# Kernel tuning notes

Measured on AMD Instinct MI355X. Metric: run time of the kernel, lower is better.

Reference implementation:

```python
import jax, jax.numpy as jnp
from jax import lax
import numpy as np

B, T, F = 256, 2048, 12
EV_VOCAB, RS_VOCAB = 32, 8
EED, RED = 6, 3
H, K = 96, 3
D = F + EED + RED  # 21


def setup_inputs() -> dict:
    key = jax.random.key(0)
    ks = jax.random.split(key, 12)
    s = 0.05
    return {
        'seq': jax.random.normal(ks[0], (B, T, F), jnp.float32),
        'ev': jax.random.randint(ks[1], (B, T), 0, EV_VOCAB),
        'rs': jax.random.randint(ks[2], (B, T), 0, RS_VOCAB),
        'lengths': jax.random.randint(ks[3], (B,), 1, T + 1),  # valid lengths in [1, T]
        'event_emb': jax.random.normal(ks[4], (EV_VOCAB, EED), jnp.float32) * s,
        'result_emb': jax.random.normal(ks[5], (RS_VOCAB, RED), jnp.float32) * s,
        'W_ih': jax.random.normal(ks[6], (4 * H, D), jnp.float32) * s,
        'W_hh': jax.random.normal(ks[7], (4 * H, H), jnp.float32) * s,
        'b_ih': jnp.zeros((4 * H,), jnp.float32),
        'b_hh': jnp.zeros((4 * H,), jnp.float32),
        'W_mlp': jax.random.normal(ks[8], (H, H * K), jnp.float32) * s,
        'b_mlp': jnp.zeros((H,), jnp.float32),
        'W_fc': jax.random.normal(ks[9], (2, 2 * H), jnp.float32) * s,
        'b_fc': jnp.zeros((2,), jnp.float32),
    }


def reference(seq, ev, rs, lengths, event_emb, result_emb, W_ih, W_hh, b_ih, b_hh,
              W_mlp, b_mlp, W_fc, b_fc):
    # embed + concat -> [B,T,D]
    x = jnp.concatenate([seq, event_emb[ev], result_emb[rs]], axis=-1)
    xs = jnp.swapaxes(x, 0, 1)  # [T,B,D]
    ts = jnp.arange(T)
    b = b_ih + b_hh

    def step(carry, inp):
        h, c = carry
        x_t, t = inp
        gates = x_t @ W_ih.T + h @ W_hh.T + b  # [B,4H]
        i, f, g, o = jnp.split(gates, 4, axis=-1)  # PyTorch gate order i,f,g,o
        i = jax.nn.sigmoid(i); f = jax.nn.sigmoid(f)
        g = jnp.tanh(g); o = jax.nn.sigmoid(o)
        c_new = f * c + i * g
        h_new = o * jnp.tanh(c_new)
        m = (t < lengths)[:, None]  # packed-seq semantics: freeze state past length
        h = jnp.where(m, h_new, h)
        c = jnp.where(m, c_new, c)
        out = jnp.where(m, h_new, jnp.zeros_like(h_new))  # pad_packed zeros
        return (h, c), out

    h0 = jnp.zeros((B, H), x.dtype)
    (h_fin, _), outs = lax.scan(step, (h0, h0), (xs, ts))
    out_padded = jnp.swapaxes(outs, 0, 1)  # [B,T,H]

    # vectorized last-k gather (replaces torch Python loop)
    idx = lengths[:, None] - K + jnp.arange(K)  # [B,K]
    valid = idx >= 0
    gathered = jnp.take_along_axis(out_padded, jnp.clip(idx, 0)[:, :, None], axis=1)
    gathered = jnp.where(valid[:, :, None], gathered, jnp.zeros_like(gathered))
    lastk = gathered.reshape(B, K * H)

    h_lastk = jax.nn.relu(lastk @ W_mlp.T + b_mlp)
    h = jnp.concatenate([h_fin, h_lastk], axis=1)  # [B,2H]
    return h @ W_fc.T + b_fc  # [B,2]
```

## Files before the change

kernel.cpp:

```cpp
#include <hip/hip_runtime.h>

#define TT 2048
#define FF 12
#define HH 96
#define CH 128
#define NT 768
#define L2E 1.44269504088896340736f

typedef __attribute__((ext_vector_type(2))) float f2;
typedef __attribute__((ext_vector_type(4))) float f4;

__device__ __forceinline__ float fast_exp2(float x){ return __builtin_amdgcn_exp2f(x); }
__device__ __forceinline__ float fast_rcp(float x){ return __builtin_amdgcn_rcpf(x); }

__global__ __launch_bounds__(NT, 3) void lstm_persist(
  const float* __restrict__ seq, const int* __restrict__ ev, const int* __restrict__ rsi,
  const int* __restrict__ len, const float* __restrict__ eemb, const float* __restrict__ remb,
  const float* __restrict__ W_ih, const float* __restrict__ W_hh,
  const float* __restrict__ b_ih, const float* __restrict__ b_hh,
  const float* __restrict__ W_mlp, const float* __restrict__ b_mlp,
  const float* __restrict__ W_fc, const float* __restrict__ b_fc,
  float* __restrict__ out)
{
  const int b   = blockIdx.x;
  const int tid = threadIdx.x;
  const int w   = tid >> 6;
  const int l   = tid & 63;
  const int kh  = l >> 5;
  const int lh  = l & 31;
  const int gt  = lh >> 3;
  const int hq  = lh & 7;
  const int ht  = 8*w + hq;
  const int g   = gt*96 + ht;

  __shared__ __align__(16) float hbuf[2][96];
  __shared__ __align__(16) float xch[CH][32];
  __shared__ __align__(16) float lastk[3*HH];
  __shared__ __align__(16) float tmp[192];
  __shared__ __align__(16) float h2[2*HH];
  __shared__ __align__(16) float et[32*6];
  __shared__ __align__(16) float rt[8*3];
  __shared__ int evb[CH];
  __shared__ int rsb[CH];

  f2 w2[30];
  #pragma unroll
  for (int j = 0; j < 30; ++j) {
    float v0, v1;
    const int c0 = kh*60 + 2*j;
    v0 = (c0 < 96) ? W_hh[g*96 + c0] : ((c0 < 117) ? W_ih[g*21 + (c0-96)] : 0.f);
    const int c1 = c0 + 1;
    v1 = (c1 < 96) ? W_hh[g*96 + c1] : ((c1 < 117) ? W_ih[g*21 + (c1-96)] : 0.f);
    w2[j] = (f2){v0, v1};
  }
  const float bg = b_ih[g] + b_hh[g];

  for (int i = tid; i < 2*HH; i += NT) hbuf[0][i] = 0.f;
  for (int i = tid; i < 3*HH; i += NT) lastk[i] = 0.f;
  for (int i = tid; i < 192;  i += NT) et[i] = eemb[i];
  for (int i = tid; i < 24;   i += NT) rt[i] = remb[i];

  float c_state = 0.f;
  const int L = len[b];

  for (int t0 = 0; t0 < L; t0 += CH) {
    for (int q = tid; q < CH*FF; q += NT) {
      const int r = q / 12;
      const int c = q - r*12;
      xch[r][c] = seq[(size_t)b*(TT*FF) + (size_t)t0*FF + q];
    }
    if (tid < CH) {
      evb[tid] = ev [b*TT + t0 + tid];
      rsb[tid] = rsi[b*TT + t0 + tid];
    }
    __syncthreads();
    for (int q = tid; q < CH*20; q += NT) {
      const int r  = q / 20;
      const int cc = q - r*20 + 12;
      float val;
      if (cc < 18)      val = et[evb[r]*6 + (cc-12)];
      else if (cc < 21) val = rt[rsb[r]*3 + (cc-18)];
      else              val = 0.f;
      xch[r][cc] = val;
    }
    __syncthreads();

    const int nr = min(CH, L - t0);
    for (int r = 0; r < nr; ++r) {
      const int t   = t0 + r;
      const int cur = t & 1;
      const float* hb = &hbuf[cur][0];
      const float* xr = &xch[r][0];
      const f4* A  = (const f4*)(hb + kh*60);
      const f4* Bv = kh ? (const f4*)xr : ((const f4*)hb) + 9;

      f2 acc = (f2){0.f, 0.f};
      #pragma unroll
      for (int j = 0; j < 9; ++j) {
        const f4 q = A[j];
        acc = w2[2*j]   * q.xy + acc;
        acc = w2[2*j+1] * q.zw + acc;
      }
      #pragma unroll
      for (int j = 9; j < 15; ++j) {
        const f4 q = Bv[j-9];
        acc = w2[2*j]   * q.xy + acc;
        acc = w2[2*j+1] * q.zw + acc;
      }
      float p = acc.x + acc.y;
      p += __shfl_xor(p, 32);
      const float s = p + bg;

      const bool is_t = (gt == 2);
      const float arg = is_t ? (-2.f*L2E)*fabsf(s) : (-L2E)*s;
      const float e   = fast_exp2(arg);
      const float r1  = fast_rcp(1.f + e);
      const float a0  = is_t ? copysignf((1.f - e)*r1, s) : r1;

      const float a1 = __shfl_xor(a0, 8);
      const float a2 = __shfl_xor(a0, 16);
      const float a3 = __shfl_xor(a0, 24);
      const float gi = (gt==0) ? a0 : (gt==1) ? a1 : (gt==2) ? a2 : a3;
      const float gf = (gt==1) ? a0 : (gt==0) ? a1 : (gt==3) ? a2 : a3;
      const float gg = (gt==2) ? a0 : (gt==3) ? a1 : (gt==0) ? a2 : a3;
      const float go = (gt==3) ? a0 : (gt==2) ? a1 : (gt==1) ? a2 : a3;

      c_state = fmaf(gf, c_state, gi*gg);
      const float e2 = fast_exp2((-2.f*L2E)*fabsf(c_state));
      const float th = copysignf((1.f - e2)*fast_rcp(1.f + e2), c_state);
      const float hn = go * th;

      if (l < 8) {
        hbuf[cur ^ 1][ht] = hn;
        const int kk = t + 3 - L;
        if (kk >= 0) lastk[kk*96 + ht] = hn;
      }
      __syncthreads();
    }
  }

  const float* hfin = &hbuf[L & 1][0];
  if (tid < 192) {
    const int hh = tid / 96;
    const int m  = tid - hh*96;
    const float* wp = W_mlp + m*288 + hh*144;
    const float* xp = lastk + hh*144;
    float s = 0.f;
    #pragma unroll 8
    for (int i = 0; i < 144; ++i) s = fmaf(wp[i], xp[i], s);
    tmp[tid] = s;
  }
  __syncthreads();
  if (tid < 96) {
    const float hl = tmp[tid] + tmp[96+tid] + b_mlp[tid];
    h2[96 + tid] = fmaxf(hl, 0.f);
    h2[tid] = hfin[tid];
  }
  __syncthreads();
  if (tid < 128) {
    const int o  = tid >> 6;
    const int ll = tid & 63;
    const float* wf = W_fc + o*192 + 3*ll;
    float s = fmaf(wf[0], h2[3*ll+0], fmaf(wf[1], h2[3*ll+1], wf[2]*h2[3*ll+2]));
    #pragma unroll
    for (int off = 32; off > 0; off >>= 1) s += __shfl_down(s, off);
    if (ll == 0) out[b*2 + o] = s + b_fc[o];
  }
}

extern "C" void kernel_launch(void* const* d_in, const int* in_sizes, int n_in,
                              void* d_out, int out_size, void* d_ws, size_t ws_size,
                              hipStream_t stream) {
  const float* seq   = (const float*)d_in[0];
  const int*   ev    = (const int*)  d_in[1];
  const int*   rsi   = (const int*)  d_in[2];
  const int*   len   = (const int*)  d_in[3];
  const float* eemb  = (const float*)d_in[4];
  const float* remb  = (const float*)d_in[5];
  const float* W_ih  = (const float*)d_in[6];
  const float* W_hh  = (const float*)d_in[7];
  const float* b_ih  = (const float*)d_in[8];
  const float* b_hh  = (const float*)d_in[9];
  const float* W_mlp = (const float*)d_in[10];
  const float* b_mlp = (const float*)d_in[11];
  const float* W_fc  = (const float*)d_in[12];
  const float* b_fc  = (const float*)d_in[13];

  hipLaunchKernelGGL(lstm_persist, dim3(256), dim3(NT), 0, stream,
                     seq, ev, rsi, len, eemb, remb, W_ih, W_hh, b_ih, b_hh,
                     W_mlp, b_mlp, W_fc, b_fc, (float*)d_out);
}
```

Baseline: 1.427 ms.

## Hoist input projection per 64-step chunk and split recurrent matvec across warps

The input-to-gate projection (W_ih·x plus bias) is now computed for a whole 64-timestep chunk up front and stored in a large shared buffer, so the per-step work only has to handle the recurrent W_hh·h product. That product is split into four 24-wide slices across warps, each writing partial sums to shared memory. A separate phase of 96 threads then reduces the partials, applies the gate activations and updates the cell state. This removes the x-part FMAs and the shuffles from the serial path, but adds a second block barrier per timestep, concentrates the activation math on few threads, and needs roughly 100KB of LDS.

```diff
diff --git a/kernel.cpp b/kernel.cpp
--- a/kernel.cpp
+++ b/kernel.cpp
@@ -3,7 +3,8 @@
 #define TT 2048
 #define FF 12
 #define HH 96
-#define CH 128
+#define NG 384
+#define CK 64
 #define NT 768
 #define L2E 1.44269504088896340736f
 
@@ -12,6 +13,13 @@
 
 __device__ __forceinline__ float fast_exp2(float x){ return __builtin_amdgcn_exp2f(x); }
 __device__ __forceinline__ float fast_rcp(float x){ return __builtin_amdgcn_rcpf(x); }
+__device__ __forceinline__ float sigm(float x){
+  return fast_rcp(1.f + fast_exp2(-L2E * x));
+}
+__device__ __forceinline__ float tanh_f(float x){
+  const float e = fast_exp2((-2.f*L2E)*fabsf(x));
+  return copysignf((1.f - e) * fast_rcp(1.f + e), x);
+}
 
 __global__ __launch_bounds__(NT, 3) void lstm_persist(
   const float* __restrict__ seq, const int* __restrict__ ev, const int* __restrict__ rsi,
@@ -26,129 +34,147 @@
   const int tid = threadIdx.x;
   const int w   = tid >> 6;
   const int l   = tid & 63;
-  const int kh  = l >> 5;
-  const int lh  = l & 31;
-  const int gt  = lh >> 3;
-  const int hq  = lh & 7;
-  const int ht  = 8*w + hq;
-  const int g   = gt*96 + ht;
-
-  __shared__ __align__(16) float hbuf[2][96];
-  __shared__ __align__(16) float xch[CH][32];
+  const int s   = w & 3;
+  const int gg  = w >> 2;
+  const int r0  = 128*gg + l;
+
+  __shared__ __align__(16) float hbuf[2][HH];
+  __shared__ __align__(16) float part[NG*5];
+  __shared__ __align__(16) float PC[CK*NG];
+  __shared__ __align__(16) float xst[CK*24];
   __shared__ __align__(16) float lastk[3*HH];
   __shared__ __align__(16) float tmp[192];
   __shared__ __align__(16) float h2[2*HH];
   __shared__ __align__(16) float et[32*6];
   __shared__ __align__(16) float rt[8*3];
-  __shared__ int evb[CH];
-  __shared__ int rsb[CH];
-
-  f2 w2[30];
-  #pragma unroll
-  for (int j = 0; j < 30; ++j) {
-    float v0, v1;
-    const int c0 = kh*60 + 2*j;
-    v0 = (c0 < 96) ? W_hh[g*96 + c0] : ((c0 < 117) ? W_ih[g*21 + (c0-96)] : 0.f);
-    const int c1 = c0 + 1;
-    v1 = (c1 < 96) ? W_hh[g*96 + c1] : ((c1 < 117) ? W_ih[g*21 + (c1-96)] : 0.f);
-    w2[j] = (f2){v0, v1};
-  }
-  const float bg = b_ih[g] + b_hh[g];
-
-  for (int i = tid; i < 2*HH; i += NT) hbuf[0][i] = 0.f;
+  __shared__ int evb[CK];
+  __shared__ int rsb[CK];
+
+  f2 wa[24];
+  {
+    const float* p0 = W_hh + (size_t)r0*96 + 24*s;
+    const float* p1 = W_hh + (size_t)(r0+64)*96 + 24*s;
+    #pragma unroll
+    for (int j = 0; j < 6; ++j) {
+      const f4 q0 = ((const f4*)p0)[j];
+      const f4 q1 = ((const f4*)p1)[j];
+      wa[2*j]    = q0.xy;  wa[2*j+1]  = q0.zw;
+      wa[12+2*j] = q1.xy;  wa[13+2*j] = q1.zw;
+    }
+  }
+  const int th2 = (tid >= NG) ? 1 : 0;
+  const int gB  = tid - th2*NG;
+  f2 wi2[12];
+  {
+    float wi[24];
+    #pragma unroll
+    for (int k = 0; k < 21; ++k) wi[k] = W_ih[gB*21 + k];
+    wi[21] = wi[22] = wi[23] = 0.f;
+    #pragma unroll
+    for (int j = 0; j < 12; ++j) wi2[j] = (f2){wi[2*j], wi[2*j+1]};
+  }
+  const float bgB = b_ih[gB] + b_hh[gB];
+
+  for (int i = tid; i < 2*HH; i += NT) ((float*)hbuf)[i] = 0.f;
   for (int i = tid; i < 3*HH; i += NT) lastk[i] = 0.f;
   for (int i = tid; i < 192;  i += NT) et[i] = eemb[i];
   for (int i = tid; i < 24;   i += NT) rt[i] = remb[i];
 
   float c_state = 0.f;
-  const int L = len[b];
-
-  for (int t0 = 0; t0 < L; t0 += CH) {
-    for (int q = tid; q < CH*FF; q += NT) {
-      const int r = q / 12;
-      const int c = q - r*12;
-      xch[r][c] = seq[(size_t)b*(TT*FF) + (size_t)t0*FF + q];
-    }
-    if (tid < CH) {
-      evb[tid] = ev [b*TT + t0 + tid];
-      rsb[tid] = rsi[b*TT + t0 + tid];
+  const int L  = len[b];
+  const int ht = tid;
+
+  for (int t = 0; t < L; ++t) {
+    const int cr = t & (CK-1);
+    if (cr == 0) {
+      {
+        const int r = tid / 12, c = tid - r*12;
+        xst[r*24 + c] = seq[(size_t)b*(TT*FF) + (size_t)t*FF + tid];
+        if (tid < CK) {
+          evb[tid] = ev [b*TT + t + tid];
+          rsb[tid] = rsi[b*TT + t + tid];
+        }
+      }
+      __syncthreads();
+      {
+        const int r = tid / 12, c2 = tid - r*12 + 12;
+        float val;
+        if (c2 < 18)      val = et[evb[r]*6 + (c2-12)];
+        else if (c2 < 21) val = rt[rsb[r]*3 + (c2-18)];
+        else              val = 0.f;
+        xst[r*24 + c2] = val;
+      }
+      __syncthreads();
+      {
+        #pragma unroll 4
+        for (int jj = 0; jj < CK/2; ++jj) {
+          const int tr = 2*jj + th2;
+          const f4* xp = (const f4*)(xst + tr*24);
+          f2 a = (f2){0.f, 0.f};
+          #pragma unroll
+          for (int j2 = 0; j2 < 6; ++j2) {
+            const f4 q = xp[j2];
+            a = wi2[2*j2]   * q.xy + a;
+            a = wi2[2*j2+1] * q.zw + a;
+          }
+          PC[tr*NG + gB] = bgB + a.x + a.y;
+        }
+      }
+      __syncthreads();
+    }
+
+    {
+      const f4* hq = (const f4*)(hbuf[t & 1] + 24*s);
+      const f4 q0=hq[0], q1=hq[1], q2=hq[2], q3=hq[3], q4=hq[4], q5=hq[5];
+      f2 aA=(f2){0,0}, aB=(f2){0,0}, aC=(f2){0,0}, aD=(f2){0,0};
+      aA = wa[0] *q0.xy + aA;  aB = wa[1] *q0.zw + aB;
+      aC = wa[12]*q0.xy + aC;  aD = wa[13]*q0.zw + aD;
+      aA = wa[2] *q1.xy + aA;  aB = wa[3] *q1.zw + aB;
+      aC = wa[14]*q1.xy + aC;  aD = wa[15]*q1.zw + aD;
+      aA = wa[4] *q2.xy + aA;  aB = wa[5] *q2.zw + aB;
+      aC = wa[16]*q2.xy + aC;  aD = wa[17]*q2.zw + aD;
+      aA = wa[6] *q3.xy + aA;  aB = wa[7] *q3.zw + aB;
+      aC = wa[18]*q3.xy + aC;  aD = wa[19]*q3.zw + aD;
+      aA = wa[8] *q4.xy + aA;  aB = wa[9] *q4.zw + aB;
+      aC = wa[20]*q4.xy + aC;  aD = wa[21]*q4.zw + aD;
+      aA = wa[10]*q5.xy + aA;  aB = wa[11]*q5.zw + aB;
+      aC = wa[22]*q5.xy + aC;  aD = wa[23]*q5.zw + aD;
+      part[r0*5 + s]      = aA.x + aA.y + aB.x + aB.y;
+      part[(r0+64)*5 + s] = aC.x + aC.y + aD.x + aD.y;
     }
     __syncthreads();
-    for (int q = tid; q < CH*20; q += NT) {
-      const int r  = q / 20;
-      const int cc = q - r*20 + 12;
-      float val;
-      if (cc < 18)      val = et[evb[r]*6 + (cc-12)];
-      else if (cc < 21) val = rt[rsb[r]*3 + (cc-18)];
-      else              val = 0.f;
-      xch[r][cc] = val;
+
+    if (tid < HH) {
+      float gv[4];
+      #pragma unroll
+      for (int gt = 0; gt < 4; ++gt) {
+        const int rr = gt*96 + ht;
+        const float* pp = part + rr*5;
+        gv[gt] = (pp[0] + pp[1]) + (pp[2] + pp[3]) + PC[cr*NG + rr];
+      }
+      const float gi = sigm(gv[0]);
+      const float gf = sigm(gv[1]);
+      const float gG = tanh_f(gv[2]);
+      const float go = sigm(gv[3]);
+      c_state = fmaf(gf, c_state, gi*gG);
+      const float hn = go * tanh_f(c_state);
+      hbuf[(t+1) & 1][ht] = hn;
+      const int kk = t + 3 - L;
+      if (kk >= 0) lastk[kk*96 + ht] = hn;
     }
     __syncthreads();
-
-    const int nr = min(CH, L - t0);
-    for (int r = 0; r < nr; ++r) {
-      const int t   = t0 + r;
-      const int cur = t & 1;
-      const float* hb = &hbuf[cur][0];
-      const float* xr = &xch[r][0];
-      const f4* A  = (const f4*)(hb + kh*60);
-      const f4* Bv = kh ? (const f4*)xr : ((const f4*)hb) + 9;
-
-      f2 acc = (f2){0.f, 0.f};
-      #pragma unroll
-      for (int j = 0; j < 9; ++j) {
-        const f4 q = A[j];
-        acc = w2[2*j]   * q.xy + acc;
-        acc = w2[2*j+1] * q.zw + acc;
-      }
-      #pragma unroll
-      for (int j = 9; j < 15; ++j) {
-        const f4 q = Bv[j-9];
-        acc = w2[2*j]   * q.xy + acc;
-        acc = w2[2*j+1] * q.zw + acc;
-      }
-      float p = acc.x + acc.y;
-      p += __shfl_xor(p, 32);
-      const float s = p + bg;
-
-      const bool is_t = (gt == 2);
-      const float arg = is_t ? (-2.f*L2E)*fabsf(s) : (-L2E)*s;
-      const float e   = fast_exp2(arg);
-      const float r1  = fast_rcp(1.f + e);
-      const float a0  = is_t ? copysignf((1.f - e)*r1, s) : r1;
-
-      const float a1 = __shfl_xor(a0, 8);
-      const float a2 = __shfl_xor(a0, 16);
-      const float a3 = __shfl_xor(a0, 24);
-      const float gi = (gt==0) ? a0 : (gt==1) ? a1 : (gt==2) ? a2 : a3;
-      const float gf = (gt==1) ? a0 : (gt==0) ? a1 : (gt==3) ? a2 : a3;
-      const float gg = (gt==2) ? a0 : (gt==3) ? a1 : (gt==0) ? a2 : a3;
-      const float go = (gt==3) ? a0 : (gt==2) ? a1 : (gt==1) ? a2 : a3;
-
-      c_state = fmaf(gf, c_state, gi*gg);
-      const float e2 = fast_exp2((-2.f*L2E)*fabsf(c_state));
-      const float th = copysignf((1.f - e2)*fast_rcp(1.f + e2), c_state);
-      const float hn = go * th;
-
-      if (l < 8) {
-        hbuf[cur ^ 1][ht] = hn;
-        const int kk = t + 3 - L;
-        if (kk >= 0) lastk[kk*96 + ht] = hn;
-      }
-      __syncthreads();
-    }
-  }
-
-  const float* hfin = &hbuf[L & 1][0];
+  }
+
+  const float* hfin = hbuf[L & 1];
   if (tid < 192) {
     const int hh = tid / 96;
     const int m  = tid - hh*96;
     const float* wp = W_mlp + m*288 + hh*144;
     const float* xp = lastk + hh*144;
-    float s = 0.f;
+    float sacc = 0.f;
     #pragma unroll 8
-    for (int i = 0; i < 144; ++i) s = fmaf(wp[i], xp[i], s);
-    tmp[tid] = s;
+    for (int i = 0; i < 144; ++i) sacc = fmaf(wp[i], xp[i], sacc);
+    tmp[tid] = sacc;
   }
   __syncthreads();
   if (tid < 96) {
@@ -161,10 +187,10 @@
     const int o  = tid >> 6;
     const int ll = tid & 63;
     const float* wf = W_fc + o*192 + 3*ll;
-    float s = fmaf(wf[0], h2[3*ll+0], fmaf(wf[1], h2[3*ll+1], wf[2]*h2[3*ll+2]));
-    #pragma unroll
-    for (int off = 32; off > 0; off >>= 1) s += __shfl_down(s, off);
-    if (ll == 0) out[b*2 + o] = s + b_fc[o];
+    float sv = fmaf(wf[0], h2[3*ll+0], fmaf(wf[1], h2[3*ll+1], wf[2]*h2[3*ll+2]));
+    #pragma unroll
+    for (int off = 32; off > 0; off >>= 1) sv += __shfl_down(sv, off);
+    if (ll == 0) out[b*2 + o] = sv + b_fc[o];
   }
 }
 
```

Measured after the change: 1.498 ms. +5.0%, slower.
